# Performance work log

Measured on AMD Instinct MI355X. Metric: run time of the kernel, lower is better.

The kernel has to match this reference:

```python
import jax, jax.numpy as jnp
import numpy as np

BETA = 0.25


def setup_inputs() -> dict:
    key = jax.random.key(0)
    k1, k2 = jax.random.split(key)
    x = jax.random.normal(k1, (4, 4096, 256), dtype=jnp.float32)
    emb = jax.random.normal(k2, (8192, 256), dtype=jnp.float32)
    return {"x": x, "emb": emb}


def reference(x, emb):
    B, C, D = x.shape
    xf = x.reshape(-1, D)  # [B*C, D]
    # squared euclidean distances (argmin-equivalent to torch.cdist p=2)
    # dist2[i, n] = ||xf_i||^2 - 2 xf_i . e_n + ||e_n||^2
    dist2 = (
        jnp.sum(xf * xf, axis=-1, keepdims=True)
        - 2.0 * jnp.einsum("td,nd->tn", xf, emb)
        + jnp.sum(emb * emb, axis=-1)[None, :]
    )  # [B*C, N]
    idx = jnp.argmin(dist2, axis=-1)  # [B*C]
    quant = emb[idx]  # [B*C, D]
    commitment_loss = jnp.mean((jax.lax.stop_gradient(quant) - xf) ** 2)
    codebook_loss = jnp.mean((quant - jax.lax.stop_gradient(xf)) ** 2)
    quantize_loss = codebook_loss + BETA * commitment_loss
    # straight-through estimator
    quant_out = xf + jax.lax.stop_gradient(quant - xf)
    quant_out = quant_out.reshape(B, C, D)
    indices = idx.reshape(B, C)
    return quant_out, quantize_loss, indices
```

## Files before the change

kernel.cpp:

```cpp
#include <hip/hip_runtime.h>
#include <stdint.h>

#define T_ROWS 16384
#define D_DIM  256
#define N_CODES 8192
#define NSPLIT 4
#define NS (N_CODES / NSPLIT)
#define NCHUNK (NS / 128)
#define NITER (NCHUNK * 8)

typedef _Float16 h8v __attribute__((ext_vector_type(8)));
typedef float f4v __attribute__((ext_vector_type(4)));
typedef unsigned short u16;
typedef unsigned int u32;
typedef unsigned long long u64;

typedef const __attribute__((address_space(1))) uint32_t* as1_t;
typedef __attribute__((address_space(3))) uint32_t* as3_t;

__device__ __forceinline__ void gload_lds16(const void* g, void* l) {
    __builtin_amdgcn_global_load_lds((as1_t)(uintptr_t)g, (as3_t)(uintptr_t)l, 16, 0, 0);
}
__device__ __forceinline__ u32 umin32(u32 a, u32 b) { return a < b ? a : b; }
__device__ __forceinline__ u32 umax32(u32 a, u32 b) { return a > b ? a : b; }

__global__ void k_prep_emb(const float* __restrict__ emb, u16* __restrict__ Ef,
                           float* __restrict__ enormP) {
    int wv = threadIdx.x >> 6, lane = threadIdx.x & 63;
    int row = blockIdx.x * 4 + wv;
    float4 v = *reinterpret_cast<const float4*>(emb + (size_t)row * D_DIM + lane * 4);
    float s = v.x * v.x + v.y * v.y + v.z * v.z + v.w * v.w;
    ushort4 h;
    { _Float16 t0=(_Float16)v.x,t1=(_Float16)v.y,t2=(_Float16)v.z,t3=(_Float16)v.w;
      h.x=*reinterpret_cast<u16*>(&t0); h.y=*reinterpret_cast<u16*>(&t1);
      h.z=*reinterpret_cast<u16*>(&t2); h.w=*reinterpret_cast<u16*>(&t3); }
    reinterpret_cast<ushort4*>(Ef + (size_t)row * D_DIM)[lane] = h;
#pragma unroll
    for (int off = 32; off; off >>= 1) s += __shfl_xor(s, off, 64);
    if (lane == 0) enormP[row] = s + 1024.0f;
}

__global__ __launch_bounds__(256, 2)
void k_main_mfma(const float* __restrict__ x, const u16* __restrict__ Ef,
                 const float* __restrict__ enormP, u32* __restrict__ cand) {
    __shared__ u16 Bs[4][4096];

    const int tid = threadIdx.x;
    const int lane = tid & 63;
    const int w = tid >> 6;
    const int c15 = lane & 15, grp = lane >> 4;
    const int m0 = (int)(blockIdx.x >> 2) * 128;
    const int split = (int)(blockIdx.x & 3);
    const int nbase = split * NS;

    int boff[8];
#pragma unroll
    for (int ni = 0; ni < 8; ++ni) {
        int r = ni * 16 + c15;
        boff[ni] = (r * 64 + grp * 16) ^ (((r >> 1) & 3) << 4);
    }
    const int srow = tid >> 2;
    const int kkb = ((tid & 3) ^ ((srow >> 1) & 3)) * 8;

    h8v a[2][8];
#pragma unroll
    for (int mi = 0; mi < 2; ++mi)
#pragma unroll
        for (int ks = 0; ks < 8; ++ks) {
            const float* p = x + (size_t)(m0 + w * 32 + mi * 16 + c15) * D_DIM + ks * 32 + grp * 8;
            float4 u0 = *reinterpret_cast<const float4*>(p);
            float4 u1 = *reinterpret_cast<const float4*>(p + 4);
            h8v av;
            av[0] = (_Float16)u0.x; av[1] = (_Float16)u0.y;
            av[2] = (_Float16)u0.z; av[3] = (_Float16)u0.w;
            av[4] = (_Float16)u1.x; av[5] = (_Float16)u1.y;
            av[6] = (_Float16)u1.z; av[7] = (_Float16)u1.w;
            a[mi][ks] = av;
        }

    auto stageB = [&](int buf, int it) {
        const int nc = it >> 3, ks = it & 7;
        const u16* src = Ef + (size_t)(nbase + nc * 128 + srow) * D_DIM + ks * 32 + kkb;
        gload_lds16(src, (char*)Bs + buf * 8192 + tid * 16);
        gload_lds16(src + 64 * D_DIM, (char*)Bs + buf * 8192 + 4096 + tid * 16);
    };

    u32 b1[8], b2[8];
#pragma unroll
    for (int l = 0; l < 8; ++l) { b1[l] = 0xFFFFFFFFu; b2[l] = 0xFFFFFFFFu; }

    stageB(0, 0);
    stageB(1, 1);
    stageB(2, 2);
    asm volatile("s_waitcnt vmcnt(4)\n\ts_barrier" ::: "memory");

    h8v bcur[8], bnxt[8];
#pragma unroll
    for (int ni = 0; ni < 8; ++ni)
        bcur[ni] = *reinterpret_cast<const h8v*>((const char*)Bs + boff[ni]);

    f4v acc[2][8];
    float en[8];

    auto do_step = [&](int it, int ks, h8v (&bc)[8], h8v (&bn)[8]) {
        asm volatile("s_waitcnt vmcnt(2)\n\ts_barrier" ::: "memory");
        {
            int it3 = it + 3;
            if (it3 > NITER - 1) it3 = NITER - 1;
            stageB((it + 3) & 3, it3);
        }
        if (ks == 0) {
            const int nc = it >> 3;
#pragma unroll
            for (int ni = 0; ni < 8; ++ni)
                en[ni] = enormP[nbase + nc * 128 + ni * 16 + c15];
        }
        {
            const char* bsb = (const char*)Bs + ((it + 1) & 3) * 8192;
#pragma unroll
            for (int ni = 0; ni < 8; ++ni)
                bn[ni] = *reinterpret_cast<const h8v*>(bsb + boff[ni]);
        }
        __builtin_amdgcn_s_setprio(1);
#pragma unroll
        for (int mi = 0; mi < 2; ++mi)
#pragma unroll
            for (int ni = 0; ni < 8; ++ni)
                acc[mi][ni] = __builtin_amdgcn_mfma_f32_16x16x32_f16(
                    a[mi][ks], bc[ni], acc[mi][ni], 0, 0, 0);
        __builtin_amdgcn_s_setprio(0);

        if (ks == 7) {
            const int nc = it >> 3;
#pragma unroll
            for (int mi = 0; mi < 2; ++mi)
#pragma unroll
                for (int r = 0; r < 4; ++r) {
                    const int l = mi * 4 + r;
                    u32 kmin = 0xFFFFFFFFu;
#pragma unroll
                    for (int ni = 0; ni < 8; ++ni) {
                        float s = fmaf(-2.0f, acc[mi][ni][r], en[ni]);
                        u32 k = (__float_as_uint(s) & 0xFFFFF800u)
                              | (u32)(nc * 128 + ni * 16 + c15);
                        kmin = umin32(kmin, k);
                    }
                    b2[l] = umin32(b2[l], umax32(b1[l], kmin));
                    b1[l] = umin32(b1[l], kmin);
                }
        }
    };

    for (int nc = 0; nc < NCHUNK; ++nc) {
#pragma unroll
        for (int mi = 0; mi < 2; ++mi)
#pragma unroll
            for (int ni = 0; ni < 8; ++ni) acc[mi][ni] = f4v{0.f, 0.f, 0.f, 0.f};

#pragma unroll
        for (int kp = 0; kp < 4; ++kp) {
            do_step(nc * 8 + kp * 2 + 0, kp * 2 + 0, bcur, bnxt);
            do_step(nc * 8 + kp * 2 + 1, kp * 2 + 1, bnxt, bcur);
        }
    }

#pragma unroll
    for (int l = 0; l < 8; ++l) {
#pragma unroll
        for (int off = 1; off < 16; off <<= 1) {
            u32 o1 = __shfl_xor(b1[l], off, 64);
            u32 o2 = __shfl_xor(b2[l], off, 64);
            b2[l] = umin32(umax32(b1[l], o1), umin32(b2[l], o2));
            b1[l] = umin32(b1[l], o1);
        }
    }
    if (c15 == 0) {
#pragma unroll
        for (int mi = 0; mi < 2; ++mi)
#pragma unroll
            for (int r = 0; r < 4; ++r) {
                const int l = mi * 4 + r;
                const int grow = m0 + w * 32 + mi * 16 + grp * 4 + r;
                cand[grow * 8 + split * 2 + 0] = (u32)nbase + (b1[l] & 0x7FFu);
                cand[grow * 8 + split * 2 + 1] = (u32)nbase + (b2[l] & 0x7FFu);
            }
    }
}

__global__ void k_refine(const float* __restrict__ x, const float* __restrict__ emb,
                         const u32* __restrict__ cand, float* __restrict__ out,
                         double* __restrict__ partials) {
    const int tid = threadIdx.x;
    const int wv = tid >> 6, lane = tid & 63;
    const int row = blockIdx.x * 4 + wv;
    const int cslot = lane >> 3, sub = lane & 7;
    int idx = (int)cand[row * 8 + cslot];
    double d = 0.0;
#pragma unroll
    for (int j = 0; j < 8; ++j) {
        float4 xv = *reinterpret_cast<const float4*>(x + (size_t)row * D_DIM + sub * 32 + j * 4);
        float4 ev = *reinterpret_cast<const float4*>(emb + (size_t)idx * D_DIM + sub * 32 + j * 4);
        double d0 = (double)xv.x - (double)ev.x;
        double d1 = (double)xv.y - (double)ev.y;
        double d2 = (double)xv.z - (double)ev.z;
        double d3 = (double)xv.w - (double)ev.w;
        d += d0 * d0 + d1 * d1 + d2 * d2 + d3 * d3;
    }
#pragma unroll
    for (int off = 1; off < 8; off <<= 1) d += __shfl_xor(d, off, 64);
#pragma unroll
    for (int off = 8; off < 64; off <<= 1) {
        double od = __shfl_xor(d, off, 64);
        int oi = __shfl_xor(idx, off, 64);
        bool better = (od < d) || (od == d && oi < idx);
        d = better ? od : d;
        idx = better ? oi : idx;
    }
    if (lane == 0) {
        out[(size_t)T_ROWS * D_DIM + 1 + row] = (float)idx;
        partials[row] = d;
    }
    float4 e = *reinterpret_cast<const float4*>(emb + (size_t)idx * D_DIM + lane * 4);
    *reinterpret_cast<float4*>(out + (size_t)row * D_DIM + lane * 4) = e;
}

__global__ void k_loss_d(const double* __restrict__ partials, float* __restrict__ out) {
    double s = 0.0;
    const int t = threadIdx.x;
#pragma unroll
    for (int i = 0; i < 64; ++i) s += partials[t + 256 * i];
#pragma unroll
    for (int off = 32; off; off >>= 1) s += __shfl_xor(s, off, 64);
    __shared__ double sm[4];
    const int wv = t >> 6, lane = t & 63;
    if (lane == 0) sm[wv] = s;
    __syncthreads();
    if (t == 0) {
        const double tot = sm[0] + sm[1] + sm[2] + sm[3];
        out[(size_t)T_ROWS * D_DIM] = (float)(1.25 * tot / (double)((size_t)T_ROWS * D_DIM));
    }
}

__global__ void k_enorm(const float* __restrict__ emb, float* __restrict__ enorm) {
    int wave = threadIdx.x >> 6, lane = threadIdx.x & 63;
    int row = blockIdx.x * 4 + wave;
    float4 v = *reinterpret_cast<const float4*>(emb + (size_t)row * D_DIM + lane * 4);
    float s = v.x * v.x + v.y * v.y + v.z * v.z + v.w * v.w;
#pragma unroll
    for (int off = 32; off; off >>= 1) s += __shfl_xor(s, off, 64);
    if (lane == 0) enorm[row] = s;
}

__global__ void k_init(u64* __restrict__ keys) {
    keys[blockIdx.x * blockDim.x + threadIdx.x] = ~0ull;
}

__global__ __launch_bounds__(256, 2)
void k_main_fp32(const float* __restrict__ x, const float* __restrict__ emb,
                 const float* __restrict__ enorm, u64* __restrict__ keys) {
    __shared__ float Xs[32][128];
    __shared__ float Es[32][128];
    __shared__ u64 red[128][16];

    const int tid = threadIdx.x;
    const int tx = tid & 15, ty = tid >> 4;
    const int m0 = (blockIdx.x >> 2) * 128;
    const int nbase = (blockIdx.x & 3) * (N_CODES / 4);

    float best[8];
    int bidx[8];
#pragma unroll
    for (int r = 0; r < 8; ++r) { best[r] = 3.4e38f; bidx[r] = 0; }

    for (int nc = 0; nc < (N_CODES / 4) / 128; ++nc) {
        const int n0 = nbase + nc * 128;
        float acc[8][8] = {};
        for (int k0 = 0; k0 < D_DIM; k0 += 32) {
            __syncthreads();
            {
                const int m = tid & 127, q = tid >> 7;
#pragma unroll
                for (int i = 0; i < 4; ++i) {
                    const int k4 = q * 4 + i * 8;
                    float4 v = *reinterpret_cast<const float4*>(
                        x + (size_t)(m0 + m) * D_DIM + k0 + k4);
                    Xs[k4 + 0][m] = v.x; Xs[k4 + 1][m] = v.y;
                    Xs[k4 + 2][m] = v.z; Xs[k4 + 3][m] = v.w;
                }
            }
            {
                const int kq = (tid & 7) * 4, nrow = tid >> 3;
#pragma unroll
                for (int i = 0; i < 4; ++i) {
                    const int n = i * 32 + nrow;
                    float4 v = *reinterpret_cast<const float4*>(
                        emb + (size_t)(n0 + n) * D_DIM + k0 + kq);
                    const int c = n ^ kq;
                    Es[kq + 0][c] = v.x; Es[kq + 1][c] = v.y;
                    Es[kq + 2][c] = v.z; Es[kq + 3][c] = v.w;
                }
            }
            __syncthreads();
#pragma unroll
            for (int kkx = 0; kkx < 32; ++kkx) {
                const int swz = kkx & 28;
                float4 xa = *reinterpret_cast<const float4*>(&Xs[kkx][ty * 4]);
                float4 xb = *reinterpret_cast<const float4*>(&Xs[kkx][64 + ty * 4]);
                const int cb = (tx * 4) ^ swz;
                float4 ea = *reinterpret_cast<const float4*>(&Es[kkx][cb]);
                float4 eb = *reinterpret_cast<const float4*>(&Es[kkx][64 + cb]);
                float xr[8] = {xa.x, xa.y, xa.z, xa.w, xb.x, xb.y, xb.z, xb.w};
                float ec[8] = {ea.x, ea.y, ea.z, ea.w, eb.x, eb.y, eb.z, eb.w};
#pragma unroll
                for (int r = 0; r < 8; ++r)
#pragma unroll
                    for (int c = 0; c < 8; ++c)
                        acc[r][c] = fmaf(xr[r], ec[c], acc[r][c]);
            }
        }
#pragma unroll
        for (int c = 0; c < 8; ++c) {
            const int ncol = n0 + ((c < 4) ? (tx * 4 + c) : (64 + tx * 4 + (c - 4)));
            const float en = enorm[ncol];
#pragma unroll
            for (int r = 0; r < 8; ++r) {
                const float score = fmaf(-2.0f, acc[r][c], en);
                if (score < best[r]) { best[r] = score; bidx[r] = ncol; }
            }
        }
    }
#pragma unroll
    for (int r = 0; r < 8; ++r) {
        const int row = (r < 4) ? (ty * 4 + r) : (64 + ty * 4 + (r - 4));
        unsigned u = __float_as_uint(best[r]);
        u = (u & 0x80000000u) ? ~u : (u | 0x80000000u);
        red[row][tx] = ((u64)u << 32) | (unsigned)bidx[r];
    }
    __syncthreads();
    if (tid < 128) {
        u64 k = red[tid][0];
#pragma unroll
        for (int t = 1; t < 16; ++t) { u64 v = red[tid][t]; k = (v < k) ? v : k; }
        atomicMin(&keys[m0 + tid], k);
    }
}

__global__ void k_out_fb(const float* __restrict__ x, const float* __restrict__ emb,
                         const u64* __restrict__ keys, float* __restrict__ out,
                         float* __restrict__ partials) {
    const int tid = threadIdx.x;
    const int m0 = blockIdx.x * 64;
    __shared__ int idx_s[64];
    if (tid < 64) {
        const u32 idx = (u32)keys[m0 + tid];
        idx_s[tid] = (int)idx;
        out[(size_t)T_ROWS * D_DIM + 1 + m0 + tid] = (float)idx;
    }
    __syncthreads();
    const int wave = tid >> 6, lane = tid & 63;
    float loss = 0.f;
#pragma unroll
    for (int i = 0; i < 16; ++i) {
        const int r = i * 4 + wave;
        const int row = m0 + r;
        const int idx = idx_s[r];
        float4 e  = *reinterpret_cast<const float4*>(emb + (size_t)idx * D_DIM + lane * 4);
        float4 xv = *reinterpret_cast<const float4*>(x + (size_t)row * D_DIM + lane * 4);
        *reinterpret_cast<float4*>(out + (size_t)row * D_DIM + lane * 4) = e;
        const float dx = e.x - xv.x, dy = e.y - xv.y, dz = e.z - xv.z, dw = e.w - xv.w;
        loss += dx * dx + dy * dy + dz * dz + dw * dw;
    }
#pragma unroll
    for (int off = 32; off; off >>= 1) loss += __shfl_xor(loss, off, 64);
    __shared__ float wl[4];
    if (lane == 0) wl[wave] = loss;
    __syncthreads();
    if (tid == 0) partials[blockIdx.x] = wl[0] + wl[1] + wl[2] + wl[3];
}

__global__ void k_loss_f(const float* __restrict__ partials, float* __restrict__ out) {
    double s = (double)partials[threadIdx.x];
#pragma unroll
    for (int off = 32; off; off >>= 1) s += __shfl_xor(s, off, 64);
    __shared__ double sm[4];
    const int wave = threadIdx.x >> 6, lane = threadIdx.x & 63;
    if (lane == 0) sm[wave] = s;
    __syncthreads();
    if (threadIdx.x == 0) {
        const double tot = sm[0] + sm[1] + sm[2] + sm[3];
        out[(size_t)T_ROWS * D_DIM] = (float)(1.25 * tot / (double)((size_t)T_ROWS * D_DIM));
    }
}

extern "C" void kernel_launch(void* const* d_in, const int* in_sizes, int n_in,
                              void* d_out, int out_size, void* d_ws, size_t ws_size,
                              hipStream_t stream) {
    const float* x = (const float*)d_in[0];
    const float* emb = (const float*)d_in[1];
    float* out = (float*)d_out;
    char* ws = (char*)d_ws;

    const size_t NEED = 4867072ull;
    if (ws_size >= NEED) {
        u16* Ef = (u16*)(ws + 0);
        float* enormP = (float*)(ws + 4194304);
        u32* cand = (u32*)(ws + 4227072);
        double* partials = (double*)(ws + 4751360);

        k_prep_emb<<<N_CODES / 4, 256, 0, stream>>>(emb, Ef, enormP);
        k_main_mfma<<<(T_ROWS / 128) * NSPLIT, 256, 0, stream>>>(x, Ef, enormP, cand);
        k_refine<<<T_ROWS / 4, 256, 0, stream>>>(x, emb, cand, out, partials);
        k_loss_d<<<1, 256, 0, stream>>>(partials, out);
    } else {
        float* enorm = (float*)(ws + 0);
        u64* keys = (u64*)(ws + 32768);
        float* partials = (float*)(ws + 163840);

        k_enorm<<<N_CODES / 4, 256, 0, stream>>>(emb, enorm);
        k_init<<<T_ROWS / 256, 256, 0, stream>>>(keys);
        k_main_fp32<<<(T_ROWS / 128) * 4, 256, 0, stream>>>(x, emb, enorm, keys);
        k_out_fb<<<T_ROWS / 64, 256, 0, stream>>>(x, emb, keys, out, partials);
        k_loss_f<<<1, 256, 0, stream>>>(partials, out);
    }
}
```

Baseline: 119.2 us.

## Retile MFMA main loop as 2x2 wave grid with LDS top-2 merge

Each wave's tile changes from 32 rows x 128 codes to 64 rows x 64 codes, so every B fragment read from LDS feeds 4 MFMAs instead of 2, halving LDS read traffic per MFMA. The register double-buffering of B fragments is removed; fragments are loaded from LDS in the same step they are used. The two column-half waves then merge their per-row top-2 candidates through a small shared array before writing. This doubles the A registers held per wave, adds a block barrier at the end, and exposes LDS latency that was hidden before.

```diff
diff --git a/kernel.cpp b/kernel.cpp
--- a/kernel.cpp
+++ b/kernel.cpp
@@ -44,30 +44,28 @@
 void k_main_mfma(const float* __restrict__ x, const u16* __restrict__ Ef,
                  const float* __restrict__ enormP, u32* __restrict__ cand) {
     __shared__ u16 Bs[4][4096];
+    __shared__ u32 topst[2][128][2];
 
     const int tid = threadIdx.x;
     const int lane = tid & 63;
     const int w = tid >> 6;
+    const int wr = w >> 1, wc = w & 1;
     const int c15 = lane & 15, grp = lane >> 4;
     const int m0 = (int)(blockIdx.x >> 2) * 128;
     const int split = (int)(blockIdx.x & 3);
     const int nbase = split * NS;
 
-    int boff[8];
-#pragma unroll
-    for (int ni = 0; ni < 8; ++ni) {
-        int r = ni * 16 + c15;
-        boff[ni] = (r * 64 + grp * 16) ^ (((r >> 1) & 3) << 4);
-    }
+    const int bbase = ((c15 * 64 + grp * 16) ^ (((c15 >> 1) & 3) << 4)) + wc * 4096;
+
     const int srow = tid >> 2;
     const int kkb = ((tid & 3) ^ ((srow >> 1) & 3)) * 8;
 
-    h8v a[2][8];
-#pragma unroll
-    for (int mi = 0; mi < 2; ++mi)
+    h8v a[4][8];
+#pragma unroll
+    for (int mi = 0; mi < 4; ++mi)
 #pragma unroll
         for (int ks = 0; ks < 8; ++ks) {
-            const float* p = x + (size_t)(m0 + w * 32 + mi * 16 + c15) * D_DIM + ks * 32 + grp * 8;
+            const float* p = x + (size_t)(m0 + wr * 64 + mi * 16 + c15) * D_DIM + ks * 32 + grp * 8;
             float4 u0 = *reinterpret_cast<const float4*>(p);
             float4 u1 = *reinterpret_cast<const float4*>(p + 4);
             h8v av;
@@ -85,105 +83,103 @@
         gload_lds16(src + 64 * D_DIM, (char*)Bs + buf * 8192 + 4096 + tid * 16);
     };
 
-    u32 b1[8], b2[8];
-#pragma unroll
-    for (int l = 0; l < 8; ++l) { b1[l] = 0xFFFFFFFFu; b2[l] = 0xFFFFFFFFu; }
+    u32 t1[16], t2[16];
+#pragma unroll
+    for (int l = 0; l < 16; ++l) { t1[l] = 0xFFFFFFFFu; t2[l] = 0xFFFFFFFFu; }
 
     stageB(0, 0);
     stageB(1, 1);
     stageB(2, 2);
-    asm volatile("s_waitcnt vmcnt(4)\n\ts_barrier" ::: "memory");
-
-    h8v bcur[8], bnxt[8];
-#pragma unroll
-    for (int ni = 0; ni < 8; ++ni)
-        bcur[ni] = *reinterpret_cast<const h8v*>((const char*)Bs + boff[ni]);
-
-    f4v acc[2][8];
-    float en[8];
-
-    auto do_step = [&](int it, int ks, h8v (&bc)[8], h8v (&bn)[8]) {
-        asm volatile("s_waitcnt vmcnt(2)\n\ts_barrier" ::: "memory");
-        {
-            int it3 = it + 3;
-            if (it3 > NITER - 1) it3 = NITER - 1;
-            stageB((it + 3) & 3, it3);
+
+    f4v acc[4][4];
+    float en[4];
+
+    for (int nc = 0; nc < NCHUNK; ++nc) {
+#pragma unroll
+        for (int mi = 0; mi < 4; ++mi)
+#pragma unroll
+            for (int ni = 0; ni < 4; ++ni) acc[mi][ni] = f4v{0.f, 0.f, 0.f, 0.f};
+
+#pragma unroll
+        for (int ks = 0; ks < 8; ++ks) {
+            const int it = nc * 8 + ks;
+            asm volatile("s_waitcnt vmcnt(2)\n\ts_barrier" ::: "memory");
+            {
+                int it3 = it + 3;
+                if (it3 > NITER - 1) it3 = NITER - 1;
+                stageB((it + 3) & 3, it3);
+            }
+            if (ks == 0) {
+#pragma unroll
+                for (int ni = 0; ni < 4; ++ni)
+                    en[ni] = enormP[nbase + nc * 128 + wc * 64 + ni * 16 + c15];
+            }
+            const char* bsb = (const char*)Bs + (it & 3) * 8192 + bbase;
+            h8v b[4];
+#pragma unroll
+            for (int ni = 0; ni < 4; ++ni)
+                b[ni] = *reinterpret_cast<const h8v*>(bsb + ni * 1024);
+
+            __builtin_amdgcn_s_setprio(1);
+#pragma unroll
+            for (int ni = 0; ni < 4; ++ni)
+#pragma unroll
+                for (int mi = 0; mi < 4; ++mi)
+                    acc[mi][ni] = __builtin_amdgcn_mfma_f32_16x16x32_f16(
+                        a[mi][ks], b[ni], acc[mi][ni], 0, 0, 0);
+            __builtin_amdgcn_s_setprio(0);
+
+            if (ks == 7) {
+#pragma unroll
+                for (int mi = 0; mi < 4; ++mi)
+#pragma unroll
+                    for (int r = 0; r < 4; ++r) {
+                        const int l = mi * 4 + r;
+                        u32 kmin = 0xFFFFFFFFu;
+#pragma unroll
+                        for (int ni = 0; ni < 4; ++ni) {
+                            float s = fmaf(-2.0f, acc[mi][ni][r], en[ni]);
+                            u32 k = (__float_as_uint(s) & 0xFFFFF800u)
+                                  | (u32)(nc * 128 + wc * 64 + ni * 16 + c15);
+                            kmin = umin32(kmin, k);
+                        }
+                        t2[l] = umin32(t2[l], umax32(t1[l], kmin));
+                        t1[l] = umin32(t1[l], kmin);
+                    }
+            }
         }
-        if (ks == 0) {
-            const int nc = it >> 3;
-#pragma unroll
-            for (int ni = 0; ni < 8; ++ni)
-                en[ni] = enormP[nbase + nc * 128 + ni * 16 + c15];
+    }
+
+#pragma unroll
+    for (int l = 0; l < 16; ++l) {
+#pragma unroll
+        for (int off = 1; off < 16; off <<= 1) {
+            u32 o1 = __shfl_xor(t1[l], off, 64);
+            u32 o2 = __shfl_xor(t2[l], off, 64);
+            t2[l] = umin32(umax32(t1[l], o1), umin32(t2[l], o2));
+            t1[l] = umin32(t1[l], o1);
         }
-        {
-            const char* bsb = (const char*)Bs + ((it + 1) & 3) * 8192;
-#pragma unroll
-            for (int ni = 0; ni < 8; ++ni)
-                bn[ni] = *reinterpret_cast<const h8v*>(bsb + boff[ni]);
-        }
-        __builtin_amdgcn_s_setprio(1);
-#pragma unroll
-        for (int mi = 0; mi < 2; ++mi)
-#pragma unroll
-            for (int ni = 0; ni < 8; ++ni)
-                acc[mi][ni] = __builtin_amdgcn_mfma_f32_16x16x32_f16(
-                    a[mi][ks], bc[ni], acc[mi][ni], 0, 0, 0);
-        __builtin_amdgcn_s_setprio(0);
-
-        if (ks == 7) {
-            const int nc = it >> 3;
-#pragma unroll
-            for (int mi = 0; mi < 2; ++mi)
-#pragma unroll
-                for (int r = 0; r < 4; ++r) {
-                    const int l = mi * 4 + r;
-                    u32 kmin = 0xFFFFFFFFu;
-#pragma unroll
-                    for (int ni = 0; ni < 8; ++ni) {
-                        float s = fmaf(-2.0f, acc[mi][ni][r], en[ni]);
-                        u32 k = (__float_as_uint(s) & 0xFFFFF800u)
-                              | (u32)(nc * 128 + ni * 16 + c15);
-                        kmin = umin32(kmin, k);
-                    }
-                    b2[l] = umin32(b2[l], umax32(b1[l], kmin));
-                    b1[l] = umin32(b1[l], kmin);
-                }
-        }
-    };
-
-    for (int nc = 0; nc < NCHUNK; ++nc) {
-#pragma unroll
-        for (int mi = 0; mi < 2; ++mi)
-#pragma unroll
-            for (int ni = 0; ni < 8; ++ni) acc[mi][ni] = f4v{0.f, 0.f, 0.f, 0.f};
-
-#pragma unroll
-        for (int kp = 0; kp < 4; ++kp) {
-            do_step(nc * 8 + kp * 2 + 0, kp * 2 + 0, bcur, bnxt);
-            do_step(nc * 8 + kp * 2 + 1, kp * 2 + 1, bnxt, bcur);
-        }
-    }
-
-#pragma unroll
-    for (int l = 0; l < 8; ++l) {
-#pragma unroll
-        for (int off = 1; off < 16; off <<= 1) {
-            u32 o1 = __shfl_xor(b1[l], off, 64);
-            u32 o2 = __shfl_xor(b2[l], off, 64);
-            b2[l] = umin32(umax32(b1[l], o1), umin32(b2[l], o2));
-            b1[l] = umin32(b1[l], o1);
-        }
     }
     if (c15 == 0) {
 #pragma unroll
-        for (int mi = 0; mi < 2; ++mi)
+        for (int mi = 0; mi < 4; ++mi)
 #pragma unroll
             for (int r = 0; r < 4; ++r) {
                 const int l = mi * 4 + r;
-                const int grow = m0 + w * 32 + mi * 16 + grp * 4 + r;
-                cand[grow * 8 + split * 2 + 0] = (u32)nbase + (b1[l] & 0x7FFu);
-                cand[grow * 8 + split * 2 + 1] = (u32)nbase + (b2[l] & 0x7FFu);
-            }
+                const int lrow = wr * 64 + mi * 16 + grp * 4 + r;
+                topst[wc][lrow][0] = t1[l];
+                topst[wc][lrow][1] = t2[l];
+            }
+    }
+    __syncthreads();
+    if (tid < 128) {
+        const u32 a1 = topst[0][tid][0], a2 = topst[0][tid][1];
+        const u32 c1 = topst[1][tid][0], c2 = topst[1][tid][1];
+        const u32 m1 = umin32(a1, c1);
+        const u32 m2 = umin32(umin32(a2, c2), umax32(a1, c1));
+        const int grow = m0 + tid;
+        cand[grow * 8 + split * 2 + 0] = (u32)nbase + (m1 & 0x7FFu);
+        cand[grow * 8 + split * 2 + 1] = (u32)nbase + (m2 & 0x7FFu);
     }
 }
 
```

New measurement: 142.5 us. 1.2x slower.

## Split codebook eight ways with triple-buffered MFMA kernel and top-2 candidate merge

Applied to the files above, without the earlier changes.

Adds a new main kernel that splits the codebook into eight slices instead of four, doubling the grid and targeting four blocks per CU with a smaller three-buffer LDS pipeline. Each block keeps a top-2 per row per slice, and a new selection kernel sorts the sixteen per-row keys to produce eight refinement candidates. The aim is more parallelism and occupancy in the distance GEMM. The cost is an extra kernel launch, extra workspace traffic, and a shallower prefetch pipeline. The path runs only when the workspace is large enough.

```diff
diff --git a/kernel.cpp b/kernel.cpp
--- a/kernel.cpp
+++ b/kernel.cpp
@@ -8,6 +8,10 @@
 #define NS (N_CODES / NSPLIT)
 #define NCHUNK (NS / 128)
 #define NITER (NCHUNK * 8)
+
+#define NS8 1024
+#define NCHUNK8 8
+#define NITER8 64
 
 typedef _Float16 h8v __attribute__((ext_vector_type(8)));
 typedef float f4v __attribute__((ext_vector_type(4)));
@@ -40,18 +44,18 @@
     if (lane == 0) enormP[row] = s + 1024.0f;
 }
 
-__global__ __launch_bounds__(256, 2)
-void k_main_mfma(const float* __restrict__ x, const u16* __restrict__ Ef,
-                 const float* __restrict__ enormP, u32* __restrict__ cand) {
-    __shared__ u16 Bs[4][4096];
+__global__ __launch_bounds__(256, 4)
+void k_main_mfma8(const float* __restrict__ x, const u16* __restrict__ Ef,
+                  const float* __restrict__ enormP, u32* __restrict__ keys2) {
+    __shared__ u16 Bs[3][4096];
 
     const int tid = threadIdx.x;
     const int lane = tid & 63;
     const int w = tid >> 6;
     const int c15 = lane & 15, grp = lane >> 4;
-    const int m0 = (int)(blockIdx.x >> 2) * 128;
-    const int split = (int)(blockIdx.x & 3);
-    const int nbase = split * NS;
+    const int m0 = (int)(blockIdx.x >> 3) * 128;
+    const int split = (int)(blockIdx.x & 7);
+    const int nbase = split * NS8;
 
     int boff[8];
 #pragma unroll
@@ -91,6 +95,176 @@
 
     stageB(0, 0);
     stageB(1, 1);
+    asm volatile("s_waitcnt vmcnt(2)\n\ts_barrier" ::: "memory");
+
+    f4v acc[2][8];
+    float en[8];
+    int rb = 0;
+
+    for (int nc = 0; nc < NCHUNK8; ++nc) {
+#pragma unroll
+        for (int ni = 0; ni < 8; ++ni)
+            en[ni] = enormP[nbase + nc * 128 + ni * 16 + c15];
+#pragma unroll
+        for (int mi = 0; mi < 2; ++mi)
+#pragma unroll
+            for (int ni = 0; ni < 8; ++ni) acc[mi][ni] = f4v{0.f, 0.f, 0.f, 0.f};
+
+#pragma unroll
+        for (int ks = 0; ks < 8; ++ks) {
+            const int it = nc * 8 + ks;
+            const int wb = rb >= 1 ? rb - 1 : 2;
+            if (it < NITER8 - 2) stageB(wb, it + 2);
+
+            h8v b[8];
+            const char* bsb = (const char*)Bs + rb * 8192;
+#pragma unroll
+            for (int ni = 0; ni < 8; ++ni)
+                b[ni] = *reinterpret_cast<const h8v*>(bsb + boff[ni]);
+
+            __builtin_amdgcn_s_setprio(1);
+#pragma unroll
+            for (int mi = 0; mi < 2; ++mi)
+#pragma unroll
+                for (int ni = 0; ni < 8; ++ni)
+                    acc[mi][ni] = __builtin_amdgcn_mfma_f32_16x16x32_f16(
+                        a[mi][ks], b[ni], acc[mi][ni], 0, 0, 0);
+            __builtin_amdgcn_s_setprio(0);
+
+            if (ks == 7) {
+#pragma unroll
+                for (int mi = 0; mi < 2; ++mi)
+#pragma unroll
+                    for (int r = 0; r < 4; ++r) {
+                        const int l = mi * 4 + r;
+                        u32 kmin = 0xFFFFFFFFu;
+#pragma unroll
+                        for (int ni = 0; ni < 8; ++ni) {
+                            float s = fmaf(-2.0f, acc[mi][ni][r], en[ni]);
+                            u32 k = (__float_as_uint(s) & 0xFFFFF800u)
+                                  | (u32)(nc * 128 + ni * 16 + c15);
+                            kmin = umin32(kmin, k);
+                        }
+                        b2[l] = umin32(b2[l], umax32(b1[l], kmin));
+                        b1[l] = umin32(b1[l], kmin);
+                    }
+            }
+
+            if (it < NITER8 - 2)
+                asm volatile("s_waitcnt vmcnt(2)\n\ts_barrier" ::: "memory");
+            else if (it == NITER8 - 2)
+                asm volatile("s_waitcnt vmcnt(0)\n\ts_barrier" ::: "memory");
+            rb = rb < 2 ? rb + 1 : 0;
+        }
+    }
+
+#pragma unroll
+    for (int l = 0; l < 8; ++l) {
+#pragma unroll
+        for (int off = 1; off < 16; off <<= 1) {
+            u32 o1 = __shfl_xor(b1[l], off, 64);
+            u32 o2 = __shfl_xor(b2[l], off, 64);
+            b2[l] = umin32(umax32(b1[l], o1), umin32(b2[l], o2));
+            b1[l] = umin32(b1[l], o1);
+        }
+    }
+    if (c15 == 0) {
+#pragma unroll
+        for (int mi = 0; mi < 2; ++mi)
+#pragma unroll
+            for (int r = 0; r < 4; ++r) {
+                const int l = mi * 4 + r;
+                const int grow = m0 + w * 32 + mi * 16 + grp * 4 + r;
+                keys2[grow * 16 + split * 2 + 0] = b1[l];
+                keys2[grow * 16 + split * 2 + 1] = b2[l];
+            }
+    }
+}
+
+__global__ void k_csel(const u32* __restrict__ keys2, u32* __restrict__ cand) {
+    const int row = blockIdx.x * 256 + threadIdx.x;
+    const uint4* p = reinterpret_cast<const uint4*>(keys2 + (size_t)row * 16);
+    u64 v[16];
+#pragma unroll
+    for (int i = 0; i < 4; ++i) {
+        uint4 q = p[i];
+        v[i * 4 + 0] = ((u64)q.x << 3) | (u32)(i * 2 + 0);
+        v[i * 4 + 1] = ((u64)q.y << 3) | (u32)(i * 2 + 0);
+        v[i * 4 + 2] = ((u64)q.z << 3) | (u32)(i * 2 + 1);
+        v[i * 4 + 3] = ((u64)q.w << 3) | (u32)(i * 2 + 1);
+    }
+#pragma unroll
+    for (int k = 2; k <= 16; k <<= 1)
+#pragma unroll
+        for (int j = k >> 1; j > 0; j >>= 1)
+#pragma unroll
+            for (int i = 0; i < 16; ++i) {
+                const int l = i ^ j;
+                if (l > i) {
+                    const bool asc = (i & k) == 0;
+                    u64 x = v[i], y = v[l];
+                    u64 lo = x < y ? x : y, hi = x < y ? y : x;
+                    v[i] = asc ? lo : hi;
+                    v[l] = asc ? hi : lo;
+                }
+            }
+#pragma unroll
+    for (int i = 0; i < 8; ++i)
+        cand[(size_t)row * 8 + i] =
+            (u32)((v[i] & 7) * 1024u + ((v[i] >> 3) & 0x3FFu));
+}
+
+__global__ __launch_bounds__(256, 2)
+void k_main_mfma(const float* __restrict__ x, const u16* __restrict__ Ef,
+                 const float* __restrict__ enormP, u32* __restrict__ cand) {
+    __shared__ u16 Bs[4][4096];
+
+    const int tid = threadIdx.x;
+    const int lane = tid & 63;
+    const int w = tid >> 6;
+    const int c15 = lane & 15, grp = lane >> 4;
+    const int m0 = (int)(blockIdx.x >> 2) * 128;
+    const int split = (int)(blockIdx.x & 3);
+    const int nbase = split * NS;
+
+    int boff[8];
+#pragma unroll
+    for (int ni = 0; ni < 8; ++ni) {
+        int r = ni * 16 + c15;
+        boff[ni] = (r * 64 + grp * 16) ^ (((r >> 1) & 3) << 4);
+    }
+    const int srow = tid >> 2;
+    const int kkb = ((tid & 3) ^ ((srow >> 1) & 3)) * 8;
+
+    h8v a[2][8];
+#pragma unroll
+    for (int mi = 0; mi < 2; ++mi)
+#pragma unroll
+        for (int ks = 0; ks < 8; ++ks) {
+            const float* p = x + (size_t)(m0 + w * 32 + mi * 16 + c15) * D_DIM + ks * 32 + grp * 8;
+            float4 u0 = *reinterpret_cast<const float4*>(p);
+            float4 u1 = *reinterpret_cast<const float4*>(p + 4);
+            h8v av;
+            av[0] = (_Float16)u0.x; av[1] = (_Float16)u0.y;
+            av[2] = (_Float16)u0.z; av[3] = (_Float16)u0.w;
+            av[4] = (_Float16)u1.x; av[5] = (_Float16)u1.y;
+            av[6] = (_Float16)u1.z; av[7] = (_Float16)u1.w;
+            a[mi][ks] = av;
+        }
+
+    auto stageB = [&](int buf, int it) {
+        const int nc = it >> 3, ks = it & 7;
+        const u16* src = Ef + (size_t)(nbase + nc * 128 + srow) * D_DIM + ks * 32 + kkb;
+        gload_lds16(src, (char*)Bs + buf * 8192 + tid * 16);
+        gload_lds16(src + 64 * D_DIM, (char*)Bs + buf * 8192 + 4096 + tid * 16);
+    };
+
+    u32 b1[8], b2[8];
+#pragma unroll
+    for (int l = 0; l < 8; ++l) { b1[l] = 0xFFFFFFFFu; b2[l] = 0xFFFFFFFFu; }
+
+    stageB(0, 0);
+    stageB(1, 1);
     stageB(2, 2);
     asm volatile("s_waitcnt vmcnt(4)\n\ts_barrier" ::: "memory");
 
@@ -400,8 +574,22 @@
     float* out = (float*)d_out;
     char* ws = (char*)d_ws;
 
-    const size_t NEED = 4867072ull;
-    if (ws_size >= NEED) {
+    const size_t NEED8 = 4194304ull + 32768 + 1048576 + 524288 + 131072;
+    const size_t NEED4 = 4194304ull + 32768 + 524288 + 131072;
+
+    if (ws_size >= NEED8) {
+        u16* Ef = (u16*)(ws + 0);
+        float* enormP = (float*)(ws + 4194304);
+        u32* keys2 = (u32*)(ws + 4227072);
+        u32* cand = (u32*)(ws + 5275648);
+        double* partials = (double*)(ws + 5799936);
+
+        k_prep_emb<<<N_CODES / 4, 256, 0, stream>>>(emb, Ef, enormP);
+        k_main_mfma8<<<(T_ROWS / 128) * 8, 256, 0, stream>>>(x, Ef, enormP, keys2);
+        k_csel<<<T_ROWS / 256, 256, 0, stream>>>(keys2, cand);
+        k_refine<<<T_ROWS / 4, 256, 0, stream>>>(x, emb, cand, out, partials);
+        k_loss_d<<<1, 256, 0, stream>>>(partials, out);
+    } else if (ws_size >= NEED4) {
         u16* Ef = (u16*)(ws + 0);
         float* enormP = (float*)(ws + 4194304);
         u32* cand = (u32*)(ws + 4227072);
```

Measured after the change: 231.7 us. 94.3% more time.

## Load codebook B-fragments directly from global memory into registers, bypassing LDS

Applied to the files above, without the earlier changes.

Adds a new main distance kernel that reads the fp16 codebook fragments straight from global memory into registers with a one-step register double buffer, replacing the LDS staging via global_load_lds and barriers. It keeps the same MFMA tiling and the top-2 candidate selection per row. This is meant to remove LDS traffic and block-wide synchronisation. In exchange, every wave fetches its own B data from global/L2 with no sharing between the four waves in a block, which raises cache traffic and leaves load latency less hidden.

```diff
diff --git a/kernel.cpp b/kernel.cpp
--- a/kernel.cpp
+++ b/kernel.cpp
@@ -41,10 +41,8 @@
 }
 
 __global__ __launch_bounds__(256, 2)
-void k_main_mfma(const float* __restrict__ x, const u16* __restrict__ Ef,
-                 const float* __restrict__ enormP, u32* __restrict__ cand) {
-    __shared__ u16 Bs[4][4096];
-
+void k_main_gs(const float* __restrict__ x, const u16* __restrict__ Ef,
+               const float* __restrict__ enormP, u32* __restrict__ cand) {
     const int tid = threadIdx.x;
     const int lane = tid & 63;
     const int w = tid >> 6;
@@ -52,15 +50,6 @@
     const int m0 = (int)(blockIdx.x >> 2) * 128;
     const int split = (int)(blockIdx.x & 3);
     const int nbase = split * NS;
-
-    int boff[8];
-#pragma unroll
-    for (int ni = 0; ni < 8; ++ni) {
-        int r = ni * 16 + c15;
-        boff[ni] = (r * 64 + grp * 16) ^ (((r >> 1) & 3) << 4);
-    }
-    const int srow = tid >> 2;
-    const int kkb = ((tid & 3) ^ ((srow >> 1) & 3)) * 8;
 
     h8v a[2][8];
 #pragma unroll
@@ -78,6 +67,132 @@
             a[mi][ks] = av;
         }
 
+    const char* EfB = (const char*)Ef;
+    u32 off = (u32)(nbase + c15) * 512u + (u32)(grp * 16);
+
+    u32 b1[8], b2[8];
+#pragma unroll
+    for (int l = 0; l < 8; ++l) { b1[l] = 0xFFFFFFFFu; b2[l] = 0xFFFFFFFFu; }
+
+    h8v bcur[8], bnxt[8];
+#pragma unroll
+    for (int ni = 0; ni < 8; ++ni)
+        bcur[ni] = *reinterpret_cast<const h8v*>(EfB + off + ni * 8192);
+
+    f4v acc[2][8];
+    float en[8];
+
+    for (int nc = 0; nc < NCHUNK; ++nc) {
+#pragma unroll
+        for (int ni = 0; ni < 8; ++ni)
+            en[ni] = enormP[nbase + nc * 128 + ni * 16 + c15];
+#pragma unroll
+        for (int mi = 0; mi < 2; ++mi)
+#pragma unroll
+            for (int ni = 0; ni < 8; ++ni) acc[mi][ni] = f4v{0.f, 0.f, 0.f, 0.f};
+
+#pragma unroll
+        for (int ks = 0; ks < 8; ++ks) {
+            h8v* bc = (ks & 1) ? bnxt : bcur;
+            h8v* bn = (ks & 1) ? bcur : bnxt;
+
+            if (ks == 7) off += 65536;
+            const int imm = (ks == 7) ? 0 : (ks + 1) * 64;
+#pragma unroll
+            for (int ni = 0; ni < 8; ++ni)
+                bn[ni] = *reinterpret_cast<const h8v*>(EfB + off + ni * 8192 + imm);
+
+            __builtin_amdgcn_s_setprio(1);
+#pragma unroll
+            for (int mi = 0; mi < 2; ++mi)
+#pragma unroll
+                for (int ni = 0; ni < 8; ++ni)
+                    acc[mi][ni] = __builtin_amdgcn_mfma_f32_16x16x32_f16(
+                        a[mi][ks], bc[ni], acc[mi][ni], 0, 0, 0);
+            __builtin_amdgcn_s_setprio(0);
+
+            if (ks == 7) {
+#pragma unroll
+                for (int mi = 0; mi < 2; ++mi)
+#pragma unroll
+                    for (int r = 0; r < 4; ++r) {
+                        const int l = mi * 4 + r;
+                        u32 kmin = 0xFFFFFFFFu;
+#pragma unroll
+                        for (int ni = 0; ni < 8; ++ni) {
+                            float s = fmaf(-2.0f, acc[mi][ni][r], en[ni]);
+                            u32 k = (__float_as_uint(s) & 0xFFFFF800u)
+                                  | (u32)(nc * 128 + ni * 16 + c15);
+                            kmin = umin32(kmin, k);
+                        }
+                        b2[l] = umin32(b2[l], umax32(b1[l], kmin));
+                        b1[l] = umin32(b1[l], kmin);
+                    }
+            }
+        }
+    }
+
+#pragma unroll
+    for (int l = 0; l < 8; ++l) {
+#pragma unroll
+        for (int o = 1; o < 16; o <<= 1) {
+            u32 o1 = __shfl_xor(b1[l], o, 64);
+            u32 o2 = __shfl_xor(b2[l], o, 64);
+            b2[l] = umin32(umax32(b1[l], o1), umin32(b2[l], o2));
+            b1[l] = umin32(b1[l], o1);
+        }
+    }
+    if (c15 == 0) {
+#pragma unroll
+        for (int mi = 0; mi < 2; ++mi)
+#pragma unroll
+            for (int r = 0; r < 4; ++r) {
+                const int l = mi * 4 + r;
+                const int grow = m0 + w * 32 + mi * 16 + grp * 4 + r;
+                cand[grow * 8 + split * 2 + 0] = (u32)nbase + (b1[l] & 0x7FFu);
+                cand[grow * 8 + split * 2 + 1] = (u32)nbase + (b2[l] & 0x7FFu);
+            }
+    }
+}
+
+__global__ __launch_bounds__(256, 2)
+void k_main_mfma(const float* __restrict__ x, const u16* __restrict__ Ef,
+                 const float* __restrict__ enormP, u32* __restrict__ cand) {
+    __shared__ u16 Bs[4][4096];
+
+    const int tid = threadIdx.x;
+    const int lane = tid & 63;
+    const int w = tid >> 6;
+    const int c15 = lane & 15, grp = lane >> 4;
+    const int m0 = (int)(blockIdx.x >> 2) * 128;
+    const int split = (int)(blockIdx.x & 3);
+    const int nbase = split * NS;
+
+    int boff[8];
+#pragma unroll
+    for (int ni = 0; ni < 8; ++ni) {
+        int r = ni * 16 + c15;
+        boff[ni] = (r * 64 + grp * 16) ^ (((r >> 1) & 3) << 4);
+    }
+    const int srow = tid >> 2;
+    const int kkb = ((tid & 3) ^ ((srow >> 1) & 3)) * 8;
+
+    h8v a[2][8];
+#pragma unroll
+    for (int mi = 0; mi < 2; ++mi)
+#pragma unroll
+        for (int ks = 0; ks < 8; ++ks) {
+            const float* p = x + (size_t)(m0 + w * 32 + mi * 16 + c15) * D_DIM + ks * 32 + grp * 8;
+            float4 u0 = *reinterpret_cast<const float4*>(p);
+            float4 u1 = *reinterpret_cast<const float4*>(p + 4);
+            h8v av;
+            av[0] = (_Float16)u0.x; av[1] = (_Float16)u0.y;
+            av[2] = (_Float16)u0.z; av[3] = (_Float16)u0.w;
+            av[4] = (_Float16)u1.x; av[5] = (_Float16)u1.y;
+            av[6] = (_Float16)u1.z; av[7] = (_Float16)u1.w;
+            a[mi][ks] = av;
+        }
+
     auto stageB = [&](int buf, int it) {
         const int nc = it >> 3, ks = it & 7;
         const u16* src = Ef + (size_t)(nbase + nc * 128 + srow) * D_DIM + ks * 32 + kkb;
@@ -408,7 +523,7 @@
         double* partials = (double*)(ws + 4751360);
 
         k_prep_emb<<<N_CODES / 4, 256, 0, stream>>>(emb, Ef, enormP);
-        k_main_mfma<<<(T_ROWS / 128) * NSPLIT, 256, 0, stream>>>(x, Ef, enormP, cand);
+        k_main_gs<<<(T_ROWS / 128) * NSPLIT, 256, 0, stream>>>(x, Ef, enormP, cand);
         k_refine<<<T_ROWS / 4, 256, 0, stream>>>(x, emb, cand, out, partials);
         k_loss_d<<<1, 256, 0, stream>>>(partials, out);
     } else {
```

Result: slower. 286.1 us (+140.0%).
